# Kernel tuning notes

Hardware: AMD Instinct MI355X
Metric: run time of the kernel (lower is better)

The kernel has to match this reference:

```python
import jax, jax.numpy as jnp
import numpy as np

DIM = 512
HEADS = 8
DIM_HEAD = 64
HIDDEN = HEADS * DIM_HEAD  # 512
SCALE = DIM_HEAD ** -0.5
EPS = 1e-12  # F.normalize default eps


def rms_norm(x, g):
    # F.normalize over channel dim (dim=1), then * g * sqrt(C)
    c = x.shape[1]
    norm = jnp.sqrt(jnp.sum(x * x, axis=1, keepdims=True))
    return x / jnp.maximum(norm, EPS) * g * (c ** 0.5)


def setup_inputs() -> dict:
    key = jax.random.key(0)
    ks = jax.random.split(key, 6)
    b, h, w = 16, 64, 64
    x = jax.random.normal(ks[0], (b, DIM, h, w), dtype=jnp.float32)
    g1 = jnp.ones((1, DIM, 1, 1), dtype=jnp.float32)
    # 1x1 conv weights stored as (out_ch, in_ch)
    Wqkv = jax.random.normal(ks[1], (HIDDEN * 3, DIM), dtype=jnp.float32) * (DIM ** -0.5)
    Wout = jax.random.normal(ks[2], (DIM, HIDDEN), dtype=jnp.float32) * (HIDDEN ** -0.5)
    bout = jax.random.normal(ks[3], (DIM,), dtype=jnp.float32) * 0.01
    g2 = jnp.ones((1, DIM, 1, 1), dtype=jnp.float32)
    return {"x": x, "g1": g1, "Wqkv": Wqkv, "Wout": Wout, "bout": bout, "g2": g2}


def reference(x, g1, Wqkv, Wout, bout, g2):
    b, c, h, w = x.shape
    n = h * w
    xn = rms_norm(x, g1)
    # 1x1 conv == channel matmul
    qkv = jnp.einsum('oc,bchw->bohw', Wqkv, xn)  # (b, 3*hidden, h, w)
    qkv = qkv.reshape(b, 3, HEADS, DIM_HEAD, n)
    q, k, v = qkv[:, 0], qkv[:, 1], qkv[:, 2]  # (b, heads, d, n)
    q = jax.nn.softmax(q, axis=-2) * SCALE      # softmax over feature dim
    k = jax.nn.softmax(k, axis=-1)               # softmax over spatial dim
    context = jnp.einsum('bhdn,bhen->bhde', k, v)  # (b,h,d,e) small
    out = jnp.einsum('bhde,bhdn->bhen', context, q)  # (b,h,e,n)
    out = out.reshape(b, HIDDEN, h, w)
    out = jnp.einsum('oc,bchw->bohw', Wout, out) + bout[None, :, None, None]
    return rms_norm(out, g2)
```

## Files before the change

### kernel.cpp

```cpp
#include <hip/hip_runtime.h>
#include <hip/hip_bf16.h>
#include <math.h>

#define B_ 16
#define C_ 512
#define N_ 4096
#define NCOL (B_ * N_)

typedef short bf16x8 __attribute__((ext_vector_type(8)));
typedef ushort ushort8_t __attribute__((ext_vector_type(8)));
typedef float f32x4 __attribute__((ext_vector_type(4)));

__device__ __forceinline__ ushort f2bf(float f) {
    unsigned u = __float_as_uint(f);
    unsigned r = (u + 0x7FFFu + ((u >> 16) & 1u)) >> 16;
    return (ushort)r;
}
__device__ __forceinline__ float bf2f(ushort u) {
    return __uint_as_float((unsigned)u << 16);
}
__device__ __forceinline__ void gload_lds16(const void* g, void* l) {
    __builtin_amdgcn_global_load_lds(
        (const __attribute__((address_space(1))) unsigned int*)g,
        (__attribute__((address_space(3))) unsigned int*)l, 16, 0, 0);
}

__global__ __launch_bounds__(256) void wprep2_k(const float* __restrict__ Wqkv,
                                                const float* __restrict__ g1,
                                                const float* __restrict__ Wout,
                                                ushort* __restrict__ Wqkvb,
                                                ushort* __restrict__ Woutb)
{
    int i = blockIdx.x * 256 + threadIdx.x;
    if (i < 196608) {
        float4 wv = reinterpret_cast<const float4*>(Wqkv)[i];
        const float4 gv = *reinterpret_cast<const float4*>(g1 + ((i * 4) & 511));
        ushort4 u;
        u.x = f2bf(wv.x * gv.x); u.y = f2bf(wv.y * gv.y);
        u.z = f2bf(wv.z * gv.z); u.w = f2bf(wv.w * gv.w);
        reinterpret_cast<ushort4*>(Wqkvb)[i] = u;
    } else {
        int j = i - 196608;
        float4 wv = reinterpret_cast<const float4*>(Wout)[j];
        ushort4 u;
        u.x = f2bf(wv.x); u.y = f2bf(wv.y); u.z = f2bf(wv.z); u.w = f2bf(wv.w);
        reinterpret_cast<ushort4*>(Woutb)[j] = u;
    }
}

__global__ __launch_bounds__(256) void transpose_k(const float* __restrict__ X,
                                                   ushort* __restrict__ Xt,
                                                   float* __restrict__ rs1)
{
    __shared__ float t[2][64][68];
    __shared__ float sr[16][64];
    const int b = blockIdx.y, n0 = blockIdx.x * 64;
    const int tid = threadIdx.x;
    const int tg = tid >> 4, tl = tid & 15;
    float sq[4] = {0.f, 0.f, 0.f, 0.f};
    for (int chunk = 0; chunk < 8; ++chunk) {
        const int buf = chunk & 1;
        const float* xp = X + ((size_t)b * C_ + chunk * 64) * N_ + n0;
        #pragma unroll
        for (int j = 0; j < 4; ++j) {
            int c = tg + j * 16;
            float4 v = *reinterpret_cast<const float4*>(xp + (size_t)c * N_ + tl * 4);
            *reinterpret_cast<float4*>(&t[buf][c][tl * 4]) = v;
            sq[0] += v.x * v.x; sq[1] += v.y * v.y;
            sq[2] += v.z * v.z; sq[3] += v.w * v.w;
        }
        __syncthreads();
        #pragma unroll
        for (int i = 0; i < 4; ++i) {
            int nl = tg + i * 16, cl = tl * 4;
            ushort4 u;
            u.x = f2bf(t[buf][cl + 0][nl]);
            u.y = f2bf(t[buf][cl + 1][nl]);
            u.z = f2bf(t[buf][cl + 2][nl]);
            u.w = f2bf(t[buf][cl + 3][nl]);
            *reinterpret_cast<ushort4*>(
                Xt + ((size_t)b * N_ + n0 + nl) * 512 + chunk * 64 + cl) = u;
        }
    }
    #pragma unroll
    for (int j = 0; j < 4; ++j) sr[tg][tl * 4 + j] = sq[j];
    __syncthreads();
    if (tid < 64) {
        float s = 0.f;
        #pragma unroll
        for (int g = 0; g < 16; ++g) s += sr[g][tid];
        rs1[(size_t)b * N_ + n0 + tid] = 22.627416998f / fmaxf(sqrtf(s), 1e-12f);
    }
}

__global__ __launch_bounds__(512, 2)
void mfma_gemm(const ushort* __restrict__ A, const ushort* __restrict__ Bt,
               const float* __restrict__ rs1,
               ushort* __restrict__ qT2, ushort* __restrict__ kd,
               ushort* __restrict__ vd)
{
    __shared__ __align__(16) char lds[2][2][32768];
    const int b  = blockIdx.z;
    const int n0 = blockIdx.x * 256;
    const int m0 = blockIdx.y * 256;
    const int tid = threadIdx.x;
    const int w = tid >> 6, l = tid & 63;
    const int wm = w >> 2, wn = w & 3;
    const int lq = l >> 4, lr = l & 15;
    const ushort* Bb = Bt + (size_t)b * N_ * 512;

    f32x4 acc[8][4];
    #pragma unroll
    for (int i = 0; i < 8; ++i)
        #pragma unroll
        for (int j = 0; j < 4; ++j)
            #pragma unroll
            for (int r = 0; r < 4; ++r) acc[i][j][r] = 0.f;

#define STAGE_STEP(t, i)                                                      \
    do {                                                                      \
        const int kb_ = (t) * 128;                                            \
        const int idx_ = (i) * 512 + tid;                                     \
        const int r_ = idx_ >> 3;                                             \
        const int ch_ = (idx_ & 7) ^ (r_ & 7);                                \
        gload_lds16((const char*)A + (size_t)(m0 + r_) * 1024 + kb_ + ch_ * 16,\
                    &lds[(t) & 1][0][idx_ * 16]);                             \
        gload_lds16((const char*)Bb + (size_t)(n0 + r_) * 1024 + kb_ + ch_ * 16,\
                    &lds[(t) & 1][1][idx_ * 16]);                             \
    } while (0)

    #pragma unroll
    for (int i = 0; i < 4; ++i) STAGE_STEP(0, i);

    bf16x8 bfr[4];
    #pragma unroll 2
    for (int t = 0; t < 8; ++t) {
        const char* As = lds[t & 1][0];
        const char* Bs = lds[t & 1][1];
        #pragma unroll
        for (int ph = 0; ph < 4; ++ph) {
            const int kk = ph >> 1, mg = ph & 1;
            bf16x8 af[4];
            if (ph != 0) {
                #pragma unroll
                for (int m2 = 0; m2 < 4; ++m2) {
                    int ra = wm * 128 + (mg * 4 + m2) * 16 + lr;
                    int ch = (kk * 4 + lq) ^ (ra & 7);
                    af[m2] = *(const bf16x8*)(As + ra * 128 + ch * 16);
                }
                if (mg == 0) {
                    #pragma unroll
                    for (int nf = 0; nf < 4; ++nf) {
                        int rb = wn * 64 + nf * 16 + lr;
                        int ch = (kk * 4 + lq) ^ (rb & 7);
                        bfr[nf] = *(const bf16x8*)(Bs + rb * 128 + ch * 16);
                    }
                }
            }
            if (t < 7) STAGE_STEP(t + 1, ph);
            if (ph == 0) {
                if (t < 7) { asm volatile("s_waitcnt vmcnt(2)" ::: "memory"); }
                else       { asm volatile("s_waitcnt vmcnt(0)" ::: "memory"); }
            }
            __builtin_amdgcn_s_barrier();
            if (ph == 0) {
                #pragma unroll
                for (int m2 = 0; m2 < 4; ++m2) {
                    int ra = wm * 128 + m2 * 16 + lr;
                    int ch = lq ^ (ra & 7);
                    af[m2] = *(const bf16x8*)(As + ra * 128 + ch * 16);
                }
                #pragma unroll
                for (int nf = 0; nf < 4; ++nf) {
                    int rb = wn * 64 + nf * 16 + lr;
                    int ch = lq ^ (rb & 7);
                    bfr[nf] = *(const bf16x8*)(Bs + rb * 128 + ch * 16);
                }
            }
            asm volatile("s_waitcnt lgkmcnt(0)" ::: "memory");
            __builtin_amdgcn_sched_barrier(0);
            __builtin_amdgcn_s_setprio(1);
            #pragma unroll
            for (int m2 = 0; m2 < 4; ++m2)
                #pragma unroll
                for (int nf = 0; nf < 4; ++nf)
                    acc[mg * 4 + m2][nf] = __builtin_amdgcn_mfma_f32_16x16x32_bf16(
                        af[m2], bfr[nf], acc[mg * 4 + m2][nf], 0, 0, 0);
            __builtin_amdgcn_s_setprio(0);
            __builtin_amdgcn_s_barrier();
        }
    }
#undef STAGE_STEP

    const int part = m0 >> 9;
    const int mloc = (m0 & 511) + wm * 128;
    const int nbase = n0 + wn * 64;
    if (part == 0) {
        #pragma unroll
        for (int hg = 0; hg < 2; ++hg) {
            const int head = (mloc >> 6) + hg;
            #pragma unroll
            for (int nf = 0; nf < 4; ++nf) {
                const int n = nbase + nf * 16 + lr;
                const float sc = rs1[(size_t)b * N_ + n];
                float v[4][4];
                float mx = -1e30f;
                #pragma unroll
                for (int m2 = 0; m2 < 4; ++m2)
                    #pragma unroll
                    for (int r = 0; r < 4; ++r) {
                        v[m2][r] = acc[hg * 4 + m2][nf][r] * sc;
                        mx = fmaxf(mx, v[m2][r]);
                    }
                mx = fmaxf(mx, __shfl_xor(mx, 16));
                mx = fmaxf(mx, __shfl_xor(mx, 32));
                float s = 0.f;
                #pragma unroll
                for (int m2 = 0; m2 < 4; ++m2)
                    #pragma unroll
                    for (int r = 0; r < 4; ++r) {
                        v[m2][r] = __expf(v[m2][r] - mx);
                        s += v[m2][r];
                    }
                s += __shfl_xor(s, 16);
                s += __shfl_xor(s, 32);
                const float r8 = 0.125f / s;
                ushort* qp = qT2 + ((size_t)b * N_ + n) * 512 + head * 64;
                #pragma unroll
                for (int m2 = 0; m2 < 4; ++m2) {
                    ushort4 u;
                    u.x = f2bf(v[m2][0] * r8);
                    u.y = f2bf(v[m2][1] * r8);
                    u.z = f2bf(v[m2][2] * r8);
                    u.w = f2bf(v[m2][3] * r8);
                    *reinterpret_cast<ushort4*>(qp + m2 * 16 + lq * 4) = u;
                }
            }
        }
    } else {
        ushort* dst = (part == 1) ? kd : vd;
        #pragma unroll
        for (int nf = 0; nf < 4; ++nf) {
            const int n = nbase + nf * 16 + lr;
            const float sc = rs1[(size_t)b * N_ + n];
            #pragma unroll
            for (int mf = 0; mf < 8; ++mf) {
                const int o = mloc + mf * 16 + lq * 4;
                #pragma unroll
                for (int r = 0; r < 4; ++r)
                    dst[((size_t)b * 512 + o + r) * N_ + n] =
                        f2bf(acc[mf][nf][r] * sc);
            }
        }
    }
}

__global__ __launch_bounds__(256) void ctx_k(const ushort* __restrict__ kk,
                                             const ushort* __restrict__ vv,
                                             float* __restrict__ ctxp,
                                             float* __restrict__ srowp)
{
    const int bh = blockIdx.x, chunk = blockIdx.y;
    const ushort* kp = kk + (size_t)bh * 64 * N_;
    const ushort* vp = vv + (size_t)bh * 64 * N_;
    __shared__ __align__(16) ushort kx[64 * 128];
    __shared__ __align__(16) ushort vx[64 * 128];
    const int tid = threadIdx.x;
    const int w = tid >> 6, l = tid & 63;
    const int lq = l >> 4, lr = l & 15;
    const int we = w >> 1, wd = w & 1;

    f32x4 acc[2][2];
    #pragma unroll
    for (int i = 0; i < 2; ++i)
        #pragma unroll
        for (int j = 0; j < 2; ++j)
            #pragma unroll
            for (int r = 0; r < 4; ++r) acc[i][j][r] = 0.f;

    float se[4] = {0.f, 0.f, 0.f, 0.f};

    for (int s = 0; s < 8; ++s) {
        const int n0 = chunk * 1024 + s * 128;
        #pragma unroll
        for (int i = 0; i < 4; ++i) {
            int idx = i * 256 + tid;
            int row = idx >> 4;
            int ch  = (idx & 15) ^ (row & 15);
            gload_lds16((const char*)(vp + (size_t)row * N_ + n0 + ch * 8),
                        (char*)vx + idx * 16);
        }
        #pragma unroll
        for (int i = 0; i < 4; ++i) {
            int idx = i * 256 + tid;
            int row = idx >> 4;
            int ch  = idx & 15;
            ushort8_t u = *reinterpret_cast<const ushort8_t*>(
                kp + (size_t)row * N_ + n0 + ch * 8);
            ushort8_t o;
            float ss = 0.f;
            #pragma unroll
            for (int t = 0; t < 8; ++t) {
                float e = __expf(bf2f(u[t]));
                ss += e;
                o[t] = f2bf(e);
            }
            se[i] += ss;
            *(ushort8_t*)((char*)kx + (row * 16 + (ch ^ (row & 15))) * 16) = o;
        }
        __syncthreads();
        #pragma unroll
        for (int k2 = 0; k2 < 4; ++k2) {
            bf16x8 af[2], bfr[2];
            #pragma unroll
            for (int i = 0; i < 2; ++i) {
                int re = we * 32 + i * 16 + lr;
                int cha = (k2 * 4 + lq) ^ (re & 15);
                af[i] = *(const bf16x8*)((const char*)vx + (re * 16 + cha) * 16);
                int rd = wd * 32 + i * 16 + lr;
                int chb = (k2 * 4 + lq) ^ (rd & 15);
                bfr[i] = *(const bf16x8*)((const char*)kx + (rd * 16 + chb) * 16);
            }
            #pragma unroll
            for (int i = 0; i < 2; ++i)
                #pragma unroll
                for (int j = 0; j < 2; ++j)
                    acc[i][j] = __builtin_amdgcn_mfma_f32_16x16x32_bf16(
                        af[i], bfr[j], acc[i][j], 0, 0, 0);
        }
        __syncthreads();
    }

    #pragma unroll
    for (int i = 0; i < 4; ++i) {
        float v = se[i];
        v += __shfl_xor(v, 1);
        v += __shfl_xor(v, 2);
        v += __shfl_xor(v, 4);
        v += __shfl_xor(v, 8);
        if (lr == 0) {
            const int row = i * 16 + w * 4 + lq;
            srowp[((size_t)bh * 4 + chunk) * 64 + row] = v;
        }
    }

    float* cbase = ctxp + ((size_t)bh * 4 + chunk) * 4096;
    #pragma unroll
    for (int j = 0; j < 2; ++j) {
        const int d = wd * 32 + j * 16 + lr;
        #pragma unroll
        for (int i = 0; i < 2; ++i) {
            const int e0 = we * 32 + i * 16 + lq * 4;
            float4 wv;
            wv.x = acc[i][j][0];
            wv.y = acc[i][j][1];
            wv.z = acc[i][j][2];
            wv.w = acc[i][j][3];
            *reinterpret_cast<float4*>(cbase + (size_t)d * 64 + e0) = wv;
        }
    }
}

__global__ __launch_bounds__(256) void wcbuild_k(const ushort* __restrict__ Wb,
                                                 const float* __restrict__ ctxp,
                                                 const float* __restrict__ srowp,
                                                 ushort* __restrict__ Wc)
{
    const int oh = blockIdx.x, h = blockIdx.y, b = blockIdx.z;
    const int bh = b * 8 + h;
    __shared__ __align__(16) ushort ws[256 * 64];
    __shared__ __align__(16) ushort cs[64 * 64];
    const int tid = threadIdx.x;
    const int w = tid >> 6, l = tid & 63;
    const int lq = l >> 4, lr = l & 15;

    #pragma unroll
    for (int i = 0; i < 8; ++i) {
        int idx = i * 256 + tid;
        int row = idx >> 3;
        int ch = (idx & 7) ^ (row & 7);
        gload_lds16(Wb + (size_t)(oh * 256 + row) * 512 + h * 64 + ch * 8,
                    (char*)ws + idx * 16);
    }
    {
        const float* cp = ctxp + (size_t)bh * 4 * 4096;
        const float* sp = srowp + (size_t)bh * 4 * 64;
        const int d = tid >> 2, eb = (tid & 3) * 16;
        const float rinv = 1.f / (sp[d] + sp[64 + d] + sp[128 + d] + sp[192 + d]);
        float vs[16];
        #pragma unroll
        for (int t4 = 0; t4 < 4; ++t4) {
            float4 a0 = *(const float4*)(cp + d * 64 + eb + t4 * 4);
            float4 a1 = *(const float4*)(cp + 4096 + d * 64 + eb + t4 * 4);
            float4 a2 = *(const float4*)(cp + 8192 + d * 64 + eb + t4 * 4);
            float4 a3 = *(const float4*)(cp + 12288 + d * 64 + eb + t4 * 4);
            vs[t4 * 4 + 0] = (a0.x + a1.x + a2.x + a3.x) * rinv;
            vs[t4 * 4 + 1] = (a0.y + a1.y + a2.y + a3.y) * rinv;
            vs[t4 * 4 + 2] = (a0.z + a1.z + a2.z + a3.z) * rinv;
            vs[t4 * 4 + 3] = (a0.w + a1.w + a2.w + a3.w) * rinv;
        }
        ushort8_t o0, o1;
        #pragma unroll
        for (int t = 0; t < 8; ++t) { o0[t] = f2bf(vs[t]); o1[t] = f2bf(vs[8 + t]); }
        const int c0 = (eb >> 3) ^ (d & 7);
        const int c1 = ((eb >> 3) + 1) ^ (d & 7);
        *(ushort8_t*)((char*)cs + (d * 8 + c0) * 16) = o0;
        *(ushort8_t*)((char*)cs + (d * 8 + c1) * 16) = o1;
    }
    __syncthreads();

    f32x4 acc[4][4];
    #pragma unroll
    for (int i = 0; i < 4; ++i)
        #pragma unroll
        for (int j = 0; j < 4; ++j)
            #pragma unroll
            for (int r = 0; r < 4; ++r) acc[i][j][r] = 0.f;

    #pragma unroll
    for (int kk = 0; kk < 2; ++kk) {
        bf16x8 af[4], bfr[4];
        #pragma unroll
        for (int mf = 0; mf < 4; ++mf) {
            int ra = w * 64 + mf * 16 + lr;
            int ch = (kk * 4 + lq) ^ (ra & 7);
            af[mf] = *(const bf16x8*)((const char*)ws + (ra * 8 + ch) * 16);
        }
        #pragma unroll
        for (int nf = 0; nf < 4; ++nf) {
            int rd = nf * 16 + lr;
            int ch = (kk * 4 + lq) ^ (rd & 7);
            bfr[nf] = *(const bf16x8*)((const char*)cs + (rd * 8 + ch) * 16);
        }
        #pragma unroll
        for (int mf = 0; mf < 4; ++mf)
            #pragma unroll
            for (int nf = 0; nf < 4; ++nf)
                acc[mf][nf] = __builtin_amdgcn_mfma_f32_16x16x32_bf16(
                    af[mf], bfr[nf], acc[mf][nf], 0, 0, 0);
    }

    ushort* wp = Wc + (size_t)b * 262144 + h * 64;
    #pragma unroll
    for (int mf = 0; mf < 4; ++mf)
        #pragma unroll
        for (int r = 0; r < 4; ++r) {
            const int o = oh * 256 + w * 64 + mf * 16 + lq * 4 + r;
            #pragma unroll
            for (int nf = 0; nf < 4; ++nf)
                wp[(size_t)o * 512 + nf * 16 + lr] = f2bf(acc[mf][nf][r]);
        }
}

__global__ __launch_bounds__(512, 2)
void gemm2_k(const ushort* __restrict__ Wc,
             const ushort* __restrict__ Bt,
             const float* __restrict__ bias,
             const float* __restrict__ g2,
             float* __restrict__ outp)
{
    __shared__ __align__(16) ushort As[512 * 64];
    __shared__ __align__(16) ushort Bs[128 * 64];
    const int b  = blockIdx.y;
    const int n0 = blockIdx.x * 128;
    const int tid = threadIdx.x;
    const int w = tid >> 6, l = tid & 63;
    const int lq = l >> 4, lr = l & 15;
    const ushort* A  = Wc + (size_t)b * 262144;
    const ushort* Bb = Bt + (size_t)b * N_ * 512;

    f32x4 acc[4][8];
    #pragma unroll
    for (int i = 0; i < 4; ++i)
        #pragma unroll
        for (int j = 0; j < 8; ++j)
            #pragma unroll
            for (int r = 0; r < 4; ++r) acc[i][j][r] = 0.f;

    for (int k0 = 0; k0 < 512; k0 += 64) {
        #pragma unroll
        for (int i = 0; i < 8; ++i) {
            int base = i * 512 + w * 64;
            int idx = base + l;
            int r = idx >> 3, ch = (idx & 7) ^ (r & 7);
            gload_lds16((const char*)A + (size_t)r * 1024 + k0 * 2 + ch * 16,
                        (char*)As + (size_t)base * 16);
        }
        #pragma unroll
        for (int i = 0; i < 2; ++i) {
            int base = i * 512 + w * 64;
            int idx = base + l;
            int r = idx >> 3, ch = (idx & 7) ^ (r & 7);
            gload_lds16((const char*)Bb + (size_t)(n0 + r) * 1024 + k0 * 2 + ch * 16,
                        (char*)Bs + (size_t)base * 16);
        }
        __syncthreads();
        #pragma unroll
        for (int kk = 0; kk < 2; ++kk) {
            bf16x8 af[4], bfv[8];
            #pragma unroll
            for (int mf = 0; mf < 4; ++mf) {
                int ra = w * 64 + mf * 16 + lr;
                int ch = (kk * 4 + lq) ^ (ra & 7);
                af[mf] = *(const bf16x8*)((const char*)As + ra * 128 + ch * 16);
            }
            #pragma unroll
            for (int nf = 0; nf < 8; ++nf) {
                int rb = nf * 16 + lr;
                int ch = (kk * 4 + lq) ^ (rb & 7);
                bfv[nf] = *(const bf16x8*)((const char*)Bs + rb * 128 + ch * 16);
            }
            #pragma unroll
            for (int mf = 0; mf < 4; ++mf)
                #pragma unroll
                for (int nf = 0; nf < 8; ++nf)
                    acc[mf][nf] = __builtin_amdgcn_mfma_f32_16x16x32_bf16(
                        af[mf], bfv[nf], acc[mf][nf], 0, 0, 0);
        }
        __syncthreads();
    }

    float4 bv[4], g2v[4];
    #pragma unroll
    for (int mf = 0; mf < 4; ++mf) {
        bv[mf]  = *reinterpret_cast<const float4*>(bias + w * 64 + mf * 16 + lq * 4);
        g2v[mf] = *reinterpret_cast<const float4*>(g2   + w * 64 + mf * 16 + lq * 4);
    }
    float csq[8] = {};
    #pragma unroll
    for (int mf = 0; mf < 4; ++mf)
        #pragma unroll
        for (int nf = 0; nf < 8; ++nf)
            #pragma unroll
            for (int r = 0; r < 4; ++r) {
                float wv = acc[mf][nf][r] + ((const float*)&bv[mf])[r];
                acc[mf][nf][r] = wv;
                csq[nf] += wv * wv;
            }
    #pragma unroll
    for (int nf = 0; nf < 8; ++nf) {
        csq[nf] += __shfl_xor(csq[nf], 16);
        csq[nf] += __shfl_xor(csq[nf], 32);
    }
    float* red  = (float*)As;
    float* rs2s = red + 1024;
    if (lq == 0) {
        #pragma unroll
        for (int nf = 0; nf < 8; ++nf)
            red[w * 128 + nf * 16 + lr] = csq[nf];
    }
    __syncthreads();
    if (tid < 128) {
        float s = 0.f;
        #pragma unroll
        for (int j = 0; j < 8; ++j) s += red[j * 128 + tid];
        rs2s[tid] = 22.627416998f / fmaxf(sqrtf(s), 1e-12f);
    }
    __syncthreads();
    #pragma unroll
    for (int nf = 0; nf < 8; ++nf) {
        const float rsv = rs2s[nf * 16 + lr];
        const int n = n0 + nf * 16 + lr;
        #pragma unroll
        for (int mf = 0; mf < 4; ++mf) {
            const int o = w * 64 + mf * 16 + lq * 4;
            float* p = outp + ((size_t)b * 512 + o) * N_ + n;
            #pragma unroll
            for (int r = 0; r < 4; ++r)
                p[(size_t)r * N_] = acc[mf][nf][r] * rsv * ((const float*)&g2v[mf])[r];
        }
    }
}

extern "C" void kernel_launch(void* const* d_in, const int* in_sizes, int n_in,
                              void* d_out, int out_size, void* d_ws, size_t ws_size,
                              hipStream_t stream)
{
    const float* x    = (const float*)d_in[0];
    const float* g1   = (const float*)d_in[1];
    const float* Wqkv = (const float*)d_in[2];
    const float* Wout = (const float*)d_in[3];
    const float* bout = (const float*)d_in[4];
    const float* g2   = (const float*)d_in[5];
    float* out = (float*)d_out;

    char* wsb = (char*)d_ws;
    ushort* qbuf  = (ushort*)wsb;
    ushort* kbuf  = (ushort*)(wsb + ((size_t)64 << 20));
    ushort* vbuf  = (ushort*)(wsb + ((size_t)128 << 20));
    ushort* Xt    = (ushort*)(wsb + ((size_t)192 << 20));
    float*  ctxp  = (float*)Xt;
    float*  srowp = (float*)(wsb + ((size_t)200 << 20));
    ushort* Wcb   = (ushort*)(wsb + ((size_t)201 << 20));
    char*   tail  = wsb + ((size_t)256 << 20);
    ushort* Wqkvb = (ushort*)tail;
    ushort* Woutb = (ushort*)(tail + (size_t)1536 * 512 * 2);
    float*  rs1   = (float*)(tail + (size_t)1536 * 512 * 2 + (size_t)512 * 512 * 2);

    wprep2_k<<<1024, 256, 0, stream>>>(Wqkv, g1, Wout, Wqkvb, Woutb);
    transpose_k<<<dim3(64, 16), 256, 0, stream>>>(x, Xt, rs1);
    mfma_gemm<<<dim3(16, 6, B_), 512, 0, stream>>>(Wqkvb, Xt, rs1,
                                                   qbuf, kbuf, vbuf);
    ctx_k<<<dim3(B_ * 8, 4), 256, 0, stream>>>(kbuf, vbuf, ctxp, srowp);
    wcbuild_k<<<dim3(2, 8, B_), 256, 0, stream>>>(Woutb, ctxp, srowp, Wcb);
    gemm2_k<<<dim3(32, B_), 512, 0, stream>>>(Wcb, qbuf, bout, g2, out);
}
```

Before: 292.9 us.

## Merge weight prep into transpose kernel and load gemm2 A operand directly from global

Fuses the weight bf16 conversion kernel into the transpose/norm kernel as extra blocks, removing one launch. In gemm2, the 512x64 A tile is no longer staged through LDS; each lane reads its bf16x8 A fragments straight from global memory, and LDS holds only the B tile plus a small reduction buffer. This shrinks LDS use (launch bound occupancy hint dropped) and removes the A LDS traffic, but A reads become uncached-per-block global loads repeated across k-steps and may add latency.

After: 298.4 us. No clear change (+1.9%).

```diff
diff --git a/kernel.cpp b/kernel.cpp
--- a/kernel.cpp
+++ b/kernel.cpp
@@ -25,37 +25,37 @@
         (__attribute__((address_space(3))) unsigned int*)l, 16, 0, 0);
 }
 
-__global__ __launch_bounds__(256) void wprep2_k(const float* __restrict__ Wqkv,
-                                                const float* __restrict__ g1,
-                                                const float* __restrict__ Wout,
-                                                ushort* __restrict__ Wqkvb,
-                                                ushort* __restrict__ Woutb)
-{
-    int i = blockIdx.x * 256 + threadIdx.x;
-    if (i < 196608) {
-        float4 wv = reinterpret_cast<const float4*>(Wqkv)[i];
-        const float4 gv = *reinterpret_cast<const float4*>(g1 + ((i * 4) & 511));
-        ushort4 u;
-        u.x = f2bf(wv.x * gv.x); u.y = f2bf(wv.y * gv.y);
-        u.z = f2bf(wv.z * gv.z); u.w = f2bf(wv.w * gv.w);
-        reinterpret_cast<ushort4*>(Wqkvb)[i] = u;
-    } else {
-        int j = i - 196608;
-        float4 wv = reinterpret_cast<const float4*>(Wout)[j];
-        ushort4 u;
-        u.x = f2bf(wv.x); u.y = f2bf(wv.y); u.z = f2bf(wv.z); u.w = f2bf(wv.w);
-        reinterpret_cast<ushort4*>(Woutb)[j] = u;
-    }
-}
-
-__global__ __launch_bounds__(256) void transpose_k(const float* __restrict__ X,
-                                                   ushort* __restrict__ Xt,
-                                                   float* __restrict__ rs1)
+__global__ __launch_bounds__(256) void prep_k(const float* __restrict__ X,
+                                              ushort* __restrict__ Xt,
+                                              float* __restrict__ rs1,
+                                              const float* __restrict__ Wqkv,
+                                              const float* __restrict__ g1,
+                                              const float* __restrict__ Wout,
+                                              ushort* __restrict__ Wqkvb,
+                                              ushort* __restrict__ Woutb)
 {
     __shared__ float t[2][64][68];
     __shared__ float sr[16][64];
-    const int b = blockIdx.y, n0 = blockIdx.x * 64;
     const int tid = threadIdx.x;
+    if (blockIdx.x >= 1024) {
+        int i = (blockIdx.x - 1024) * 256 + tid;
+        if (i < 196608) {
+            float4 wv = reinterpret_cast<const float4*>(Wqkv)[i];
+            const float4 gv = *reinterpret_cast<const float4*>(g1 + ((i * 4) & 511));
+            ushort4 u;
+            u.x = f2bf(wv.x * gv.x); u.y = f2bf(wv.y * gv.y);
+            u.z = f2bf(wv.z * gv.z); u.w = f2bf(wv.w * gv.w);
+            reinterpret_cast<ushort4*>(Wqkvb)[i] = u;
+        } else {
+            int j = i - 196608;
+            float4 wv = reinterpret_cast<const float4*>(Wout)[j];
+            ushort4 u;
+            u.x = f2bf(wv.x); u.y = f2bf(wv.y); u.z = f2bf(wv.z); u.w = f2bf(wv.w);
+            reinterpret_cast<ushort4*>(Woutb)[j] = u;
+        }
+        return;
+    }
+    const int b = blockIdx.x >> 6, n0 = (blockIdx.x & 63) * 64;
     const int tg = tid >> 4, tl = tid & 15;
     float sq[4] = {0.f, 0.f, 0.f, 0.f};
     for (int chunk = 0; chunk < 8; ++chunk) {
@@ -452,21 +452,22 @@
         }
 }
 
-__global__ __launch_bounds__(512, 2)
+__global__ __launch_bounds__(512)
 void gemm2_k(const ushort* __restrict__ Wc,
              const ushort* __restrict__ Bt,
              const float* __restrict__ bias,
              const float* __restrict__ g2,
              float* __restrict__ outp)
 {
-    __shared__ __align__(16) ushort As[512 * 64];
     __shared__ __align__(16) ushort Bs[128 * 64];
+    __shared__ float red[1152];
     const int b  = blockIdx.y;
     const int n0 = blockIdx.x * 128;
     const int tid = threadIdx.x;
     const int w = tid >> 6, l = tid & 63;
     const int lq = l >> 4, lr = l & 15;
-    const ushort* A  = Wc + (size_t)b * 262144;
+    const ushort* Alane = Wc + (size_t)b * 262144 +
+                          (size_t)(w * 64 + lr) * 512 + lq * 8;
     const ushort* Bb = Bt + (size_t)b * N_ * 512;
 
     f32x4 acc[4][8];
@@ -478,14 +479,6 @@
             for (int r = 0; r < 4; ++r) acc[i][j][r] = 0.f;
 
     for (int k0 = 0; k0 < 512; k0 += 64) {
-        #pragma unroll
-        for (int i = 0; i < 8; ++i) {
-            int base = i * 512 + w * 64;
-            int idx = base + l;
-            int r = idx >> 3, ch = (idx & 7) ^ (r & 7);
-            gload_lds16((const char*)A + (size_t)r * 1024 + k0 * 2 + ch * 16,
-                        (char*)As + (size_t)base * 16);
-        }
         #pragma unroll
         for (int i = 0; i < 2; ++i) {
             int base = i * 512 + w * 64;
@@ -499,11 +492,9 @@
         for (int kk = 0; kk < 2; ++kk) {
             bf16x8 af[4], bfv[8];
             #pragma unroll
-            for (int mf = 0; mf < 4; ++mf) {
-                int ra = w * 64 + mf * 16 + lr;
-                int ch = (kk * 4 + lq) ^ (ra & 7);
-                af[mf] = *(const bf16x8*)((const char*)As + ra * 128 + ch * 16);
-            }
+            for (int mf = 0; mf < 4; ++mf)
+                af[mf] = *reinterpret_cast<const bf16x8*>(
+                    Alane + (size_t)mf * 16 * 512 + k0 + kk * 32);
             #pragma unroll
             for (int nf = 0; nf < 8; ++nf) {
                 int rb = nf * 16 + lr;
@@ -542,7 +533,6 @@
         csq[nf] += __shfl_xor(csq[nf], 16);
         csq[nf] += __shfl_xor(csq[nf], 32);
     }
-    float* red  = (float*)As;
     float* rs2s = red + 1024;
     if (lq == 0) {
         #pragma unroll
@@ -597,8 +587,7 @@
     ushort* Woutb = (ushort*)(tail + (size_t)1536 * 512 * 2);
     float*  rs1   = (float*)(tail + (size_t)1536 * 512 * 2 + (size_t)512 * 512 * 2);
 
-    wprep2_k<<<1024, 256, 0, stream>>>(Wqkv, g1, Wout, Wqkvb, Woutb);
-    transpose_k<<<dim3(64, 16), 256, 0, stream>>>(x, Xt, rs1);
+    prep_k<<<2048, 256, 0, stream>>>(x, Xt, rs1, Wqkv, g1, Wout, Wqkvb, Woutb);
     mfma_gemm<<<dim3(16, 6, B_), 512, 0, stream>>>(Wqkvb, Xt, rs1,
                                                    qbuf, kbuf, vbuf);
     ctx_k<<<dim3(B_ * 8, 4), 256, 0, stream>>>(kbuf, vbuf, ctxp, srowp);
```
